# Kernel optimization log

Measured on AMD Instinct MI355X. Metric: run time of the kernel, lower is better.

The kernel has to match this reference:

```python
import jax, jax.numpy as jnp
import numpy as np

D_MODEL = 256
SELF_NHEAD = 8
ATT_NHEAD = 8
DFF = 1024
H2D, W2D = 40, 40
MAX_DIS = 7
WS = 2 * MAX_DIS + 1  # 15x15 local window
LOCAL_DIL = 1
GN_GROUPS = 32
EPS = 1e-5


def _ln(x, g, b):
    m = jnp.mean(x, -1, keepdims=True)
    v = jnp.var(x, -1, keepdims=True)
    return (x - m) * jax.lax.rsqrt(v + EPS) * g + b


def _mha_core(q, k, v, nh):
    # q,k,v: (L, B, C); Q scaled by 1/sqrt(head_dim) as in AOT MultiheadAttention
    Lq, B, C = q.shape
    hd = C // nh
    qh = (q / jnp.asarray(hd ** 0.5, q.dtype)).reshape(Lq, B, nh, hd).transpose(1, 2, 0, 3)
    kh = k.reshape(-1, B, nh, hd).transpose(1, 2, 0, 3)
    vh = v.reshape(-1, B, nh, hd).transpose(1, 2, 0, 3)
    attn = jax.nn.softmax(jnp.einsum('bhqd,bhkd->bhqk', qh, kh), axis=-1)
    o = jnp.einsum('bhqk,bhkd->bhqd', attn, vh)
    return o.transpose(2, 0, 1, 3).reshape(Lq, B, C)


def _unfold(x, ws, dil):
    # x: (N, C, H, W) -> (N, C, ws*ws, H, W) local windows (zero-padded)
    n, c, h, w = x.shape
    p = (ws // 2) * dil
    pat = jax.lax.conv_general_dilated_patches(
        x, (ws, ws), (1, 1), [(p, p), (p, p)], rhs_dilation=(dil, dil))
    return pat.reshape(n, c, ws * ws, h, w)


def _local_attn(q2, k2, v2, nh, ws, dil):
    # q2,k2,v2: (B, C, H, W); windowed attention over (2*max_dis+1)^2 neighborhood
    b, c, h, w = q2.shape
    hd = c // nh
    qh = (q2 / jnp.asarray(hd ** 0.5, q2.dtype)).reshape(b, nh, hd, h * w)
    uk = _unfold(k2, ws, dil).reshape(b, nh, hd, ws * ws, h * w)
    uv = _unfold(v2, ws, dil).reshape(b, nh, hd, ws * ws, h * w)
    valid = _unfold(jnp.ones((1, 1, h, w), q2.dtype), ws, dil).reshape(1, 1, ws * ws, h * w) > 0.5
    logits = jnp.einsum('bhdn,bhdwn->bhwn', qh, uk)
    logits = jnp.where(valid, logits, jnp.asarray(-1e9, logits.dtype))
    attn = jax.nn.softmax(logits, axis=2)
    o = jnp.einsum('bhwn,bhdwn->bhdn', attn, uv)
    return o.reshape(b, c, h * w).transpose(2, 0, 1)  # (HW, B, C)


def _seq_to_2d(x, h, w):
    l, b, c = x.shape
    return x.reshape(h, w, b, c).transpose(2, 3, 0, 1)  # (B, C, h, w)


def _block(tgt, curr_id_emb, self_pos,
           ln1_g, ln1_b, sa_wq, sa_bq, sa_wk, sa_bk, sa_wv, sa_bv, sa_wo, sa_bo,
           ln2_g, ln2_b, w_qv, b_qv, w_id, b_id, lt_wo, lt_bo, st_wo, st_bo,
           ln3_g, ln3_b, w1, b1, gn_g, gn_b, dw_k, w2, b2):
    h, w = H2D, W2D
    # --- self attention (global_dilation == 1) ---
    _t = _ln(tgt, ln1_g, ln1_b)
    qk_in = _t + self_pos
    q_ = qk_in @ sa_wq.T + sa_bq
    k_ = qk_in @ sa_wk.T + sa_bk
    v_ = _t @ sa_wv.T + sa_bv
    tgt2 = _mha_core(q_, k_, v_, SELF_NHEAD) @ sa_wo.T + sa_bo
    tgt = tgt + tgt2
    # --- QV projection + ID-gated KV fusion ---
    _t = _ln(tgt, ln2_g, ln2_b)
    qv = _t @ w_qv.T + b_qv
    curr_Q = qv[..., :D_MODEL]  # curr_K == curr_Q
    curr_V = qv[..., D_MODEL:]
    id_kv = curr_id_emb @ w_id.T + b_id
    id_k = id_kv[..., :ATT_NHEAD]
    id_v = id_kv[..., ATT_NHEAD:]
    L, B, C = curr_Q.shape
    hd = C // ATT_NHEAD
    global_K = (curr_Q.reshape(L, B, ATT_NHEAD, hd) * (1.0 + jnp.tanh(id_k))[..., None]).reshape(L, B, C)
    global_V = curr_V + id_v
    # --- long-term (global) attention, no input linear ---
    tgt2 = _mha_core(curr_Q, global_K, global_V, ATT_NHEAD) @ lt_wo.T + lt_bo
    # --- short-term (local windowed) attention ---
    lq = _seq_to_2d(curr_Q, h, w)
    lk = _seq_to_2d(global_K, h, w)
    lv = _seq_to_2d(global_V, h, w)
    tgt3 = _local_attn(lq, lk, lv, ATT_NHEAD, WS, LOCAL_DIL) @ st_wo.T + st_bo
    tgt = tgt + tgt2 + tgt3
    # --- FFN with GN + GELU + depthwise 5x5 conv (GNActDWConv2d) ---
    _t = _ln(tgt, ln3_g, ln3_b)
    x = _t @ w1.T + b1  # (L, B, DFF)
    x2 = _seq_to_2d(x, h, w)  # (B, DFF, h, w)
    xr = x2.reshape(B, GN_GROUPS, DFF // GN_GROUPS, h, w)
    m = xr.mean((2, 3, 4), keepdims=True)
    va = xr.var((2, 3, 4), keepdims=True)
    x2 = ((xr - m) * jax.lax.rsqrt(va + EPS)).reshape(B, DFF, h, w)
    x2 = x2 * gn_g[None, :, None, None] + gn_b[None, :, None, None]
    x2 = jax.nn.gelu(x2, approximate=False)
    x2 = jax.lax.conv_general_dilated(
        x2, dw_k, (1, 1), [(2, 2), (2, 2)], feature_group_count=DFF,
        dimension_numbers=('NCHW', 'OIHW', 'NCHW'))
    x = x2.reshape(B, DFF, h * w).transpose(2, 0, 1)
    tgt2 = x @ w2.T + b2
    return tgt + tgt2


def setup_inputs() -> dict:
    key = jax.random.key(0)
    ks = jax.random.split(key, 40)
    L = H2D * W2D
    B = 1
    C = D_MODEL
    w = lambda k, s: jax.random.normal(k, s, jnp.float32) * 0.02
    inp = {
        'tgt': jax.random.normal(ks[0], (L, B, C), jnp.float32),
        'curr_id_emb': jax.random.normal(ks[1], (L, B, C), jnp.float32),
        'self_pos': jax.random.normal(ks[2], (L, B, C), jnp.float32),
        'ln1_g': jnp.ones((C,), jnp.float32), 'ln1_b': jnp.zeros((C,), jnp.float32),
        'sa_wq': w(ks[3], (C, C)), 'sa_bq': jnp.zeros((C,), jnp.float32),
        'sa_wk': w(ks[4], (C, C)), 'sa_bk': jnp.zeros((C,), jnp.float32),
        'sa_wv': w(ks[5], (C, C)), 'sa_bv': jnp.zeros((C,), jnp.float32),
        'sa_wo': w(ks[6], (C, C)), 'sa_bo': jnp.zeros((C,), jnp.float32),
        'ln2_g': jnp.ones((C,), jnp.float32), 'ln2_b': jnp.zeros((C,), jnp.float32),
        'w_qv': w(ks[7], (2 * C, C)), 'b_qv': jnp.zeros((2 * C,), jnp.float32),
        'w_id': w(ks[8], (C + ATT_NHEAD, C)), 'b_id': jnp.zeros((C + ATT_NHEAD,), jnp.float32),
        'lt_wo': w(ks[9], (C, C)), 'lt_bo': jnp.zeros((C,), jnp.float32),
        'st_wo': w(ks[10], (C, C)), 'st_bo': jnp.zeros((C,), jnp.float32),
        'ln3_g': jnp.ones((C,), jnp.float32), 'ln3_b': jnp.zeros((C,), jnp.float32),
        'w1': w(ks[11], (DFF, C)), 'b1': jnp.zeros((DFF,), jnp.float32),
        'gn_g': jnp.ones((DFF,), jnp.float32), 'gn_b': jnp.zeros((DFF,), jnp.float32),
        'dw_k': w(ks[12], (DFF, 1, 5, 5)),
        'w2': w(ks[13], (C, DFF)), 'b2': jnp.zeros((C,), jnp.float32),
    }
    return inp


def reference(tgt, curr_id_emb, self_pos,
              ln1_g, ln1_b, sa_wq, sa_bq, sa_wk, sa_bk, sa_wv, sa_bv, sa_wo, sa_bo,
              ln2_g, ln2_b, w_qv, b_qv, w_id, b_id, lt_wo, lt_bo, st_wo, st_bo,
              ln3_g, ln3_b, w1, b1, gn_g, gn_b, dw_k, w2, b2):
    return _block(tgt, curr_id_emb, self_pos,
                  ln1_g, ln1_b, sa_wq, sa_bq, sa_wk, sa_bk, sa_wv, sa_bv, sa_wo, sa_bo,
                  ln2_g, ln2_b, w_qv, b_qv, w_id, b_id, lt_wo, lt_bo, st_wo, st_bo,
                  ln3_g, ln3_b, w1, b1, gn_g, gn_b, dw_k, w2, b2)
```

## Files before the change

### kernel.cpp

```cpp
#include <hip/hip_runtime.h>
#include <math.h>

#define L_SEQ 1600
#define CDIM 256
#define NH 8
#define HD 32
#define GRID_H 40
#define GRID_W 40
#define DFF_ 1024
#define SCALE_QK 0.17677669529663687f

typedef __attribute__((ext_vector_type(8))) short short8;
typedef __attribute__((ext_vector_type(4))) float f32x4;

__device__ __forceinline__ float waveReduceSum(float v) {
#pragma unroll
    for (int off = 32; off > 0; off >>= 1) v += __shfl_down(v, off, 64);
    return v;
}
__device__ __forceinline__ float blockReduceSum(float v, float* sh4) {
    v = waveReduceSum(v);
    int lane = threadIdx.x & 63, wid = threadIdx.x >> 6;
    __syncthreads();
    if (lane == 0) sh4[wid] = v;
    __syncthreads();
    return sh4[0] + sh4[1] + sh4[2] + sh4[3];
}

__device__ __forceinline__ unsigned short f2bf(float x) {
    union { float f; unsigned u; } v; v.f = x;
    unsigned r = (v.u + 0x7FFFu + ((v.u >> 16) & 1u)) >> 16;
    return (unsigned short)r;
}
__device__ __forceinline__ unsigned pkbf(float lo, float hi) {
    return (unsigned)f2bf(lo) | ((unsigned)f2bf(hi) << 16);
}

__global__ __launch_bounds__(256) void ln_kernel(const float* __restrict__ x,
                                                 const float* __restrict__ g,
                                                 const float* __restrict__ b,
                                                 const float* __restrict__ addin,
                                                 float* __restrict__ out,
                                                 float* __restrict__ out2) {
    __shared__ float sh4[4];
    int row = blockIdx.x;
    int c = threadIdx.x;
    float v = x[row * CDIM + c];
    float mean = blockReduceSum(v, sh4) * (1.0f / CDIM);
    float d = v - mean;
    float var = blockReduceSum(d * d, sh4) * (1.0f / CDIM);
    float y = d * rsqrtf(var + 1e-5f) * g[c] + b[c];
    out[row * CDIM + c] = y;
    if (out2) out2[row * CDIM + c] = y + addin[row * CDIM + c];
}

struct GJob {
    const float* A; const float* W; const float* bias; const float* res;
    float* C; int N; int K;
};

__global__ __launch_bounds__(256) void gemm_mfma(GJob j0, GJob j1, GJob j2) {
    GJob j = j0;
    if (blockIdx.z == 1) j = j1;
    else if (blockIdx.z == 2) j = j2;
    const float* __restrict__ A = j.A;
    const float* __restrict__ W = j.W;
    const float* bias = j.bias;
    const float* res = j.res;
    float* __restrict__ C = j.C;
    int N = j.N, K = j.K;

    __shared__ unsigned short Al[2][4][64][8];
    __shared__ unsigned short Bl[2][4][64][8];
    int tid = threadIdx.x;
    int bm = blockIdx.y * 64, bn = blockIdx.x * 64;
    if (bn >= N) return;
    int lane = tid & 63, wave = tid >> 6;
    int wr = wave >> 1, wc = wave & 1;

    int srow = tid >> 3;
    int q = tid & 7;
    int e0 = (q & 1) * 4;

    f32x4 acc[2][2] = {};
    int nsteps = K >> 5;

    float4 ra[2], rb[2];
    {
#pragma unroll
        for (int r = 0; r < 2; ++r) {
            int row = srow + 32 * r;
            ra[r] = *(const float4*)(A + (bm + row) * K + 4 * q);
            int n = bn + row;
            rb[r] = (n < N) ? *(const float4*)(W + n * K + 4 * q)
                            : make_float4(0.f, 0.f, 0.f, 0.f);
        }
#pragma unroll
        for (int r = 0; r < 2; ++r) {
            int row = srow + 32 * r;
            int frag = (row >> 4), l = (row & 15) + 16 * (q >> 1);
            *(uint2*)&Al[0][frag][l][e0] = make_uint2(pkbf(ra[r].x, ra[r].y), pkbf(ra[r].z, ra[r].w));
            *(uint2*)&Bl[0][frag][l][e0] = make_uint2(pkbf(rb[r].x, rb[r].y), pkbf(rb[r].z, rb[r].w));
        }
    }
    __syncthreads();

    for (int s = 0; s < nsteps; ++s) {
        bool more = (s + 1) < nsteps;
        if (more) {
            int k0 = (s + 1) << 5;
#pragma unroll
            for (int r = 0; r < 2; ++r) {
                int row = srow + 32 * r;
                ra[r] = *(const float4*)(A + (bm + row) * K + k0 + 4 * q);
                int n = bn + row;
                rb[r] = (n < N) ? *(const float4*)(W + n * K + k0 + 4 * q)
                                : make_float4(0.f, 0.f, 0.f, 0.f);
            }
        }
        {
            int buf = s & 1;
            short8 af[2], bfr[2];
#pragma unroll
            for (int i = 0; i < 2; ++i) {
                af[i] = *(const short8*)&Al[buf][2 * wr + i][lane][0];
                bfr[i] = *(const short8*)&Bl[buf][2 * wc + i][lane][0];
            }
#pragma unroll
            for (int i = 0; i < 2; ++i)
#pragma unroll
                for (int jj = 0; jj < 2; ++jj)
                    acc[i][jj] = __builtin_amdgcn_mfma_f32_16x16x32_bf16(af[i], bfr[jj], acc[i][jj], 0, 0, 0);
        }
        if (more) {
            int buf = (s + 1) & 1;
#pragma unroll
            for (int r = 0; r < 2; ++r) {
                int row = srow + 32 * r;
                int frag = (row >> 4), l = (row & 15) + 16 * (q >> 1);
                *(uint2*)&Al[buf][frag][l][e0] = make_uint2(pkbf(ra[r].x, ra[r].y), pkbf(ra[r].z, ra[r].w));
                *(uint2*)&Bl[buf][frag][l][e0] = make_uint2(pkbf(rb[r].x, rb[r].y), pkbf(rb[r].z, rb[r].w));
            }
        }
        __syncthreads();
    }

#pragma unroll
    for (int jj = 0; jj < 2; ++jj) {
        int col = bn + wc * 32 + jj * 16 + (lane & 15);
        if (col >= N) continue;
        float bv = bias ? bias[col] : 0.f;
#pragma unroll
        for (int i = 0; i < 2; ++i) {
            int rbase = bm + wr * 32 + i * 16 + ((lane >> 4) << 2);
#pragma unroll
            for (int r = 0; r < 4; ++r) {
                int row = rbase + r;
                float v = acc[i][jj][r] + bv;
                if (res) v += res[row * N + col];
                C[row * N + col] = v;
            }
        }
    }
}

#define QBLK 32
#define KTJ 128
__global__ __launch_bounds__(256) void mha_mfma(const float* __restrict__ Q, int ldq,
                                                const float* __restrict__ K, int ldk,
                                                const float* __restrict__ V, int ldv,
                                                const float* __restrict__ idkv,
                                                float* __restrict__ O, int ldo) {
    __shared__ unsigned short Kl[8][64][8];
    __shared__ unsigned short Vl[4][2][64][12];
    __shared__ float mred[4][2][16];
    __shared__ float lred[4][2][16];
    __shared__ float Osh[3][2][2][64][4];
    int h = blockIdx.y;
    int qbase = blockIdx.x * QBLK;
    int tid = threadIdx.x;
    int w = tid >> 6, lane = tid & 63;
    int g = lane >> 4, c = lane & 15;

    short8 qfrag[2];
#pragma unroll
    for (int qt = 0; qt < 2; ++qt) {
        const float* qp = Q + (qbase + qt * 16 + c) * ldq + h * HD + g * 8;
        float4 f0 = *(const float4*)qp;
        float4 f1 = *(const float4*)(qp + 4);
        short8 s;
        s[0] = (short)f2bf(f0.x * SCALE_QK); s[1] = (short)f2bf(f0.y * SCALE_QK);
        s[2] = (short)f2bf(f0.z * SCALE_QK); s[3] = (short)f2bf(f0.w * SCALE_QK);
        s[4] = (short)f2bf(f1.x * SCALE_QK); s[5] = (short)f2bf(f1.y * SCALE_QK);
        s[6] = (short)f2bf(f1.z * SCALE_QK); s[7] = (short)f2bf(f1.w * SCALE_QK);
        qfrag[qt] = s;
    }

    float m[2] = { -INFINITY, -INFINITY };
    float l[2] = { 0.f, 0.f };
    f32x4 acc_o[2][2] = {};

    int jrow = tid >> 1;
    int dhalf = (tid & 1) * 16;
    int vjq = tid >> 3;
    int vdq = tid & 7;
    int vjr = 4 * vjq;
    int vd0 = 4 * vdq;
    int vjc = vjr >> 5, vdt = vd0 >> 4, vjg = (vjr & 31) >> 3, ve0 = vjr & 7;

    int src_lo = 16 * ((2 * g) & 3) + c;
    int src_hi = 16 * ((2 * g + 1) & 3) + c;
    bool hisel = (g >= 2);

    for (int t = 0; t < L_SEQ; t += KTJ) {
        {
            int jj = t + jrow;
            float4 f0, f1, f2, f3;
            if (jj < L_SEQ) {
                const float4* kp = (const float4*)(K + jj * ldk + h * HD + dhalf);
                f0 = kp[0]; f1 = kp[1]; f2 = kp[2]; f3 = kp[3];
                if (idkv) {
                    float gt = 1.f + tanhf(idkv[jj * 264 + h]);
                    f0.x *= gt; f0.y *= gt; f0.z *= gt; f0.w *= gt;
                    f1.x *= gt; f1.y *= gt; f1.z *= gt; f1.w *= gt;
                    f2.x *= gt; f2.y *= gt; f2.z *= gt; f2.w *= gt;
                    f3.x *= gt; f3.y *= gt; f3.z *= gt; f3.w *= gt;
                }
            } else {
                f0 = f1 = f2 = f3 = make_float4(0.f, 0.f, 0.f, 0.f);
            }
            int jt = jrow >> 4;
            int laneA = (jrow & 15) + dhalf * 2;
            short8 s0, s1;
            s0[0]=f2bf(f0.x); s0[1]=f2bf(f0.y); s0[2]=f2bf(f0.z); s0[3]=f2bf(f0.w);
            s0[4]=f2bf(f1.x); s0[5]=f2bf(f1.y); s0[6]=f2bf(f1.z); s0[7]=f2bf(f1.w);
            s1[0]=f2bf(f2.x); s1[1]=f2bf(f2.y); s1[2]=f2bf(f2.z); s1[3]=f2bf(f2.w);
            s1[4]=f2bf(f3.x); s1[5]=f2bf(f3.y); s1[6]=f2bf(f3.z); s1[7]=f2bf(f3.w);
            *(short8*)&Kl[jt][laneA][0] = s0;
            *(short8*)&Kl[jt][laneA + 16][0] = s1;
        }
        {
            float4 rr[4];
            int j0 = t + vjr;
#pragma unroll
            for (int r = 0; r < 4; ++r) {
                int jj = j0 + r;
                if (jj < L_SEQ) {
                    float4 fv = *(const float4*)(V + jj * ldv + h * HD + vd0);
                    if (idkv) {
                        float4 av = *(const float4*)(idkv + jj * 264 + 8 + h * HD + vd0);
                        fv.x += av.x; fv.y += av.y; fv.z += av.z; fv.w += av.w;
                    }
                    rr[r] = fv;
                } else {
                    rr[r] = make_float4(0.f, 0.f, 0.f, 0.f);
                }
            }
            float col[4][4] = {
                { rr[0].x, rr[1].x, rr[2].x, rr[3].x },
                { rr[0].y, rr[1].y, rr[2].y, rr[3].y },
                { rr[0].z, rr[1].z, rr[2].z, rr[3].z },
                { rr[0].w, rr[1].w, rr[2].w, rr[3].w } };
#pragma unroll
            for (int dd = 0; dd < 4; ++dd) {
                int laneV = ((vd0 + dd) & 15) + 16 * vjg;
                uint2 pk;
                pk.x = pkbf(col[dd][0], col[dd][1]);
                pk.y = pkbf(col[dd][2], col[dd][3]);
                *(uint2*)&Vl[vjc][vdt][laneV][ve0] = pk;
            }
        }
        __syncthreads();

        bool alive = (t + 32 * w) < L_SEQ;
        if (alive) {
            short8 kf0 = *(const short8*)&Kl[2 * w][lane][0];
            short8 kf1 = *(const short8*)&Kl[2 * w + 1][lane][0];
            f32x4 zero = { 0.f, 0.f, 0.f, 0.f };
            f32x4 s[2][2];
            s[0][0] = __builtin_amdgcn_mfma_f32_16x16x32_bf16(kf0, qfrag[0], zero, 0, 0, 0);
            s[0][1] = __builtin_amdgcn_mfma_f32_16x16x32_bf16(kf0, qfrag[1], zero, 0, 0, 0);
            s[1][0] = __builtin_amdgcn_mfma_f32_16x16x32_bf16(kf1, qfrag[0], zero, 0, 0, 0);
            s[1][1] = __builtin_amdgcn_mfma_f32_16x16x32_bf16(kf1, qfrag[1], zero, 0, 0, 0);

            short8 pfrag[2];
#pragma unroll
            for (int qt = 0; qt < 2; ++qt) {
                float mx = s[0][qt][0];
                mx = fmaxf(mx, s[0][qt][1]); mx = fmaxf(mx, s[0][qt][2]); mx = fmaxf(mx, s[0][qt][3]);
                mx = fmaxf(mx, s[1][qt][0]); mx = fmaxf(mx, s[1][qt][1]);
                mx = fmaxf(mx, s[1][qt][2]); mx = fmaxf(mx, s[1][qt][3]);
                mx = fmaxf(mx, __shfl_xor(mx, 16, 64));
                mx = fmaxf(mx, __shfl_xor(mx, 32, 64));
                float nm = fmaxf(m[qt], mx);
                float alpha = __expf(m[qt] - nm);
                m[qt] = nm;
                float p00 = __expf(s[0][qt][0] - nm), p01 = __expf(s[0][qt][1] - nm);
                float p02 = __expf(s[0][qt][2] - nm), p03 = __expf(s[0][qt][3] - nm);
                float p10 = __expf(s[1][qt][0] - nm), p11 = __expf(s[1][qt][1] - nm);
                float p12 = __expf(s[1][qt][2] - nm), p13 = __expf(s[1][qt][3] - nm);
                float ts = ((p00 + p01) + (p02 + p03)) + ((p10 + p11) + (p12 + p13));
                ts += __shfl_xor(ts, 16, 64);
                ts += __shfl_xor(ts, 32, 64);
                l[qt] = l[qt] * alpha + ts;
#pragma unroll
                for (int dt = 0; dt < 2; ++dt) {
                    acc_o[dt][qt][0] *= alpha; acc_o[dt][qt][1] *= alpha;
                    acc_o[dt][qt][2] *= alpha; acc_o[dt][qt][3] *= alpha;
                }
                unsigned w00 = pkbf(p00, p01), w01 = pkbf(p02, p03);
                unsigned w10 = pkbf(p10, p11), w11 = pkbf(p12, p13);
                unsigned a0 = __shfl(w00, src_lo, 64);
                unsigned a1 = __shfl(w10, src_lo, 64);
                unsigned b0 = __shfl(w01, src_lo, 64);
                unsigned b1 = __shfl(w11, src_lo, 64);
                unsigned c0 = __shfl(w00, src_hi, 64);
                unsigned c1 = __shfl(w10, src_hi, 64);
                unsigned d0 = __shfl(w01, src_hi, 64);
                unsigned d1 = __shfl(w11, src_hi, 64);
                union { short8 s8; unsigned u[4]; } P;
                P.u[0] = hisel ? a1 : a0;
                P.u[1] = hisel ? b1 : b0;
                P.u[2] = hisel ? c1 : c0;
                P.u[3] = hisel ? d1 : d0;
                pfrag[qt] = P.s8;
            }

            union { short8 s8; uint2 v[2]; } vf0u, vf1u;
            vf0u.v[0] = *(const uint2*)&Vl[w][0][lane][0];
            vf0u.v[1] = *(const uint2*)&Vl[w][0][lane][4];
            vf1u.v[0] = *(const uint2*)&Vl[w][1][lane][0];
            vf1u.v[1] = *(const uint2*)&Vl[w][1][lane][4];
            acc_o[0][0] = __builtin_amdgcn_mfma_f32_16x16x32_bf16(vf0u.s8, pfrag[0], acc_o[0][0], 0, 0, 0);
            acc_o[0][1] = __builtin_amdgcn_mfma_f32_16x16x32_bf16(vf0u.s8, pfrag[1], acc_o[0][1], 0, 0, 0);
            acc_o[1][0] = __builtin_amdgcn_mfma_f32_16x16x32_bf16(vf1u.s8, pfrag[0], acc_o[1][0], 0, 0, 0);
            acc_o[1][1] = __builtin_amdgcn_mfma_f32_16x16x32_bf16(vf1u.s8, pfrag[1], acc_o[1][1], 0, 0, 0);
        }
        __syncthreads();
    }

    if (g == 0) {
#pragma unroll
        for (int qt = 0; qt < 2; ++qt) { mred[w][qt][c] = m[qt]; lred[w][qt][c] = l[qt]; }
    }
    if (w > 0) {
#pragma unroll
        for (int dt = 0; dt < 2; ++dt)
#pragma unroll
            for (int qt = 0; qt < 2; ++qt)
                *(f32x4*)&Osh[w - 1][dt][qt][lane][0] = acc_o[dt][qt];
    }
    __syncthreads();
    if (w == 0) {
#pragma unroll
        for (int qt = 0; qt < 2; ++qt) {
            float m0_ = mred[0][qt][c], m1_ = mred[1][qt][c];
            float m2_ = mred[2][qt][c], m3_ = mred[3][qt][c];
            float M = fmaxf(fmaxf(m0_, m1_), fmaxf(m2_, m3_));
            float a0 = __expf(m0_ - M), a1 = __expf(m1_ - M);
            float a2 = __expf(m2_ - M), a3 = __expf(m3_ - M);
            float L = a0 * lred[0][qt][c] + a1 * lred[1][qt][c]
                    + a2 * lred[2][qt][c] + a3 * lred[3][qt][c];
            float inv = 1.f / L;
#pragma unroll
            for (int dt = 0; dt < 2; ++dt) {
                f32x4 o1 = *(const f32x4*)&Osh[0][dt][qt][lane][0];
                f32x4 o2 = *(const f32x4*)&Osh[1][dt][qt][lane][0];
                f32x4 o3 = *(const f32x4*)&Osh[2][dt][qt][lane][0];
                float4 r;
                r.x = (acc_o[dt][qt][0] * a0 + o1[0] * a1 + o2[0] * a2 + o3[0] * a3) * inv;
                r.y = (acc_o[dt][qt][1] * a0 + o1[1] * a1 + o2[1] * a2 + o3[1] * a3) * inv;
                r.z = (acc_o[dt][qt][2] * a0 + o1[2] * a1 + o2[2] * a2 + o3[2] * a3) * inv;
                r.w = (acc_o[dt][qt][3] * a0 + o1[3] * a1 + o2[3] * a2 + o3[3] * a3) * inv;
                *(float4*)(O + (qbase + qt * 16 + c) * ldo + h * HD + dt * 16 + 4 * g) = r;
            }
        }
    }
}

__global__ __launch_bounds__(256, 1) void local_mfma(const float* __restrict__ Q, int ldq,
                                                     const float* __restrict__ K, int ldk,
                                                     const float* __restrict__ V, int ldv,
                                                     const float* __restrict__ idkv,
                                                     float* __restrict__ O, int ldo) {
    __shared__ unsigned short Kp[768 * 40];
    __shared__ unsigned short Vt[32 * 776];
    __shared__ float mred[4][3][16];
    __shared__ float lred[4][3][16];
    __shared__ float Osh[3][2][3][64][4];
    int y = blockIdx.x, h = blockIdx.y;
    int tid = threadIdx.x;
    int w = tid >> 6, lane = tid & 63;
    int g = lane >> 4, c = lane & 15;

#pragma unroll 4
    for (int rep = 0; rep < 24; ++rep) {
        int idx = rep * 256 + tid;
        int key = idx >> 3, dq = idx & 7;
        int ky = key / 48;
        int xx = key - 48 * ky;
        int yy = y + ky - 7;
        bool ok = (xx < 40) && (yy >= 0) && (yy < 40);
        float4 fk = make_float4(0.f, 0.f, 0.f, 0.f);
        float4 fv = make_float4(0.f, 0.f, 0.f, 0.f);
        if (ok) {
            int row = yy * 40 + xx;
            fk = *(const float4*)(K + row * ldk + h * HD + 4 * dq);
            fv = *(const float4*)(V + row * ldv + h * HD + 4 * dq);
            if (idkv) {
                float gt = 1.f + tanhf(idkv[row * 264 + h]);
                fk.x *= gt; fk.y *= gt; fk.z *= gt; fk.w *= gt;
                float4 av = *(const float4*)(idkv + row * 264 + 8 + h * HD + 4 * dq);
                fv.x += av.x; fv.y += av.y; fv.z += av.z; fv.w += av.w;
            }
        }
        *(uint2*)&Kp[key * 40 + 4 * dq] = make_uint2(pkbf(fk.x, fk.y), pkbf(fk.z, fk.w));
        int vb = (4 * dq) * 776 + key;
        Vt[vb] = f2bf(fv.x);
        Vt[vb + 776] = f2bf(fv.y);
        Vt[vb + 1552] = f2bf(fv.z);
        Vt[vb + 2328] = f2bf(fv.w);
    }

    short8 qfrag[3];
#pragma unroll
    for (int qt = 0; qt < 3; ++qt) {
        short8 s = { 0, 0, 0, 0, 0, 0, 0, 0 };
        int qx = qt * 16 + c;
        if (qx < 40) {
            const float* qp = Q + (y * 40 + qx) * ldq + h * HD + g * 8;
            float4 f0 = *(const float4*)qp;
            float4 f1 = *(const float4*)(qp + 4);
            s[0] = (short)f2bf(f0.x * SCALE_QK); s[1] = (short)f2bf(f0.y * SCALE_QK);
            s[2] = (short)f2bf(f0.z * SCALE_QK); s[3] = (short)f2bf(f0.w * SCALE_QK);
            s[4] = (short)f2bf(f1.x * SCALE_QK); s[5] = (short)f2bf(f1.y * SCALE_QK);
            s[6] = (short)f2bf(f1.z * SCALE_QK); s[7] = (short)f2bf(f1.w * SCALE_QK);
        }
        qfrag[qt] = s;
    }
    __syncthreads();

    f32x4 sfr[12][3];
    const f32x4 zf = { 0.f, 0.f, 0.f, 0.f };
#pragma unroll
    for (int i = 0; i < 12; ++i) {
        int ky = 4 * w + i / 3;
        int fx = i % 3;
        short8 kf = *(const short8*)&Kp[(ky * 48 + fx * 16 + c) * 40 + 8 * g];
#pragma unroll
        for (int qt = 0; qt < 3; ++qt)
            sfr[i][qt] = __builtin_amdgcn_mfma_f32_16x16x32_bf16(kf, qfrag[qt], zf, 0, 0, 0);
    }

    float mw[3] = { -1e30f, -1e30f, -1e30f };
#pragma unroll
    for (int i = 0; i < 12; ++i) {
        int ky = 4 * w + i / 3, fx = i % 3;
        int yy = y + ky - 7;
        bool rowok = (yy >= 0) && (yy < 40);
        int xxb = fx * 16 + 4 * g;
#pragma unroll
        for (int qt = 0; qt < 3; ++qt) {
            int qx = qt * 16 + c;
#pragma unroll
            for (int r = 0; r < 4; ++r) {
                int xx = xxb + r;
                int dd = xx - qx;
                bool ok = rowok && (xx < 40) && (dd <= 7) && (dd >= -7);
                float v = ok ? sfr[i][qt][r] : -1e9f;
                sfr[i][qt][r] = v;
                mw[qt] = fmaxf(mw[qt], v);
            }
        }
    }
#pragma unroll
    for (int qt = 0; qt < 3; ++qt) {
        mw[qt] = fmaxf(mw[qt], __shfl_xor(mw[qt], 16, 64));
        mw[qt] = fmaxf(mw[qt], __shfl_xor(mw[qt], 32, 64));
    }
    if (lane < 16) {
#pragma unroll
        for (int qt = 0; qt < 3; ++qt) mred[w][qt][lane] = mw[qt];
    }
    __syncthreads();
    float M[3];
#pragma unroll
    for (int qt = 0; qt < 3; ++qt)
        M[qt] = fmaxf(fmaxf(mred[0][qt][c], mred[1][qt][c]),
                      fmaxf(mred[2][qt][c], mred[3][qt][c]));

    float lsum[3] = { 0.f, 0.f, 0.f };
    f32x4 acc_o[2][3] = {};
    int src_lo = 16 * ((2 * g) & 3) + c;
    int src_hi = 16 * ((2 * g + 1) & 3) + c;
    bool hisel = (g >= 2);
#pragma unroll
    for (int chk = 0; chk < 6; ++chk) {
        short8 pfrag[3];
#pragma unroll
        for (int qt = 0; qt < 3; ++qt) {
            float p00 = __expf(sfr[2 * chk][qt][0] - M[qt]);
            float p01 = __expf(sfr[2 * chk][qt][1] - M[qt]);
            float p02 = __expf(sfr[2 * chk][qt][2] - M[qt]);
            float p03 = __expf(sfr[2 * chk][qt][3] - M[qt]);
            float p10 = __expf(sfr[2 * chk + 1][qt][0] - M[qt]);
            float p11 = __expf(sfr[2 * chk + 1][qt][1] - M[qt]);
            float p12 = __expf(sfr[2 * chk + 1][qt][2] - M[qt]);
            float p13 = __expf(sfr[2 * chk + 1][qt][3] - M[qt]);
            lsum[qt] += ((p00 + p01) + (p02 + p03)) + ((p10 + p11) + (p12 + p13));
            unsigned w00 = pkbf(p00, p01), w01 = pkbf(p02, p03);
            unsigned w10 = pkbf(p10, p11), w11 = pkbf(p12, p13);
            unsigned a0 = __shfl(w00, src_lo, 64);
            unsigned a1 = __shfl(w10, src_lo, 64);
            unsigned b0 = __shfl(w01, src_lo, 64);
            unsigned b1 = __shfl(w11, src_lo, 64);
            unsigned c0 = __shfl(w00, src_hi, 64);
            unsigned c1 = __shfl(w10, src_hi, 64);
            unsigned d0 = __shfl(w01, src_hi, 64);
            unsigned d1 = __shfl(w11, src_hi, 64);
            union { short8 s8; unsigned u[4]; } P;
            P.u[0] = hisel ? a1 : a0;
            P.u[1] = hisel ? b1 : b0;
            P.u[2] = hisel ? c1 : c0;
            P.u[3] = hisel ? d1 : d0;
            pfrag[qt] = P.s8;
        }
        int jb = 32 * (6 * w + chk);
        short8 vf0 = *(const short8*)&Vt[c * 776 + jb + 8 * g];
        short8 vf1 = *(const short8*)&Vt[(16 + c) * 776 + jb + 8 * g];
#pragma unroll
        for (int qt = 0; qt < 3; ++qt) {
            acc_o[0][qt] = __builtin_amdgcn_mfma_f32_16x16x32_bf16(vf0, pfrag[qt], acc_o[0][qt], 0, 0, 0);
            acc_o[1][qt] = __builtin_amdgcn_mfma_f32_16x16x32_bf16(vf1, pfrag[qt], acc_o[1][qt], 0, 0, 0);
        }
    }

#pragma unroll
    for (int qt = 0; qt < 3; ++qt) {
        lsum[qt] += __shfl_xor(lsum[qt], 16, 64);
        lsum[qt] += __shfl_xor(lsum[qt], 32, 64);
    }
    if (lane < 16) {
#pragma unroll
        for (int qt = 0; qt < 3; ++qt) lred[w][qt][lane] = lsum[qt];
    }
    if (w > 0) {
#pragma unroll
        for (int dt = 0; dt < 2; ++dt)
#pragma unroll
            for (int qt = 0; qt < 3; ++qt)
                *(f32x4*)&Osh[w - 1][dt][qt][lane][0] = acc_o[dt][qt];
    }
    __syncthreads();
    if (w == 0) {
#pragma unroll
        for (int qt = 0; qt < 3; ++qt) {
            int qx = qt * 16 + c;
            if (qx >= 40) continue;
            float L = (lred[0][qt][c] + lred[1][qt][c]) + (lred[2][qt][c] + lred[3][qt][c]);
            float inv = 1.f / L;
#pragma unroll
            for (int dt = 0; dt < 2; ++dt) {
                f32x4 o1 = *(const f32x4*)&Osh[0][dt][qt][lane][0];
                f32x4 o2 = *(const f32x4*)&Osh[1][dt][qt][lane][0];
                f32x4 o3 = *(const f32x4*)&Osh[2][dt][qt][lane][0];
                float4 r;
                r.x = (acc_o[dt][qt][0] + o1[0] + o2[0] + o3[0]) * inv;
                r.y = (acc_o[dt][qt][1] + o1[1] + o2[1] + o3[1]) * inv;
                r.z = (acc_o[dt][qt][2] + o1[2] + o2[2] + o3[2]) * inv;
                r.w = (acc_o[dt][qt][3] + o1[3] + o2[3] + o3[3]) * inv;
                *(float4*)(O + (y * 40 + qx) * ldo + h * HD + dt * 16 + 4 * g) = r;
            }
        }
    }
}

__global__ __launch_bounds__(256) void prep_misc(const float* __restrict__ Kw,
                                                 const float* __restrict__ lt_wo,
                                                 const float* __restrict__ lt_bo,
                                                 const float* __restrict__ st_wo,
                                                 const float* __restrict__ st_bo,
                                                 float* __restrict__ Kt,
                                                 float* __restrict__ wcat,
                                                 float* __restrict__ bsum) {
    int idx = blockIdx.x * 256 + threadIdx.x;
    int n = idx >> 8, k = idx & 255;
    wcat[n * 512 + k] = lt_wo[idx];
    wcat[n * 512 + 256 + k] = st_wo[idx];
    if (idx < 256) bsum[idx] = lt_bo[idx] + st_bo[idx];
    if (idx < 25 * DFF_) {
        int kk = idx >> 10, c = idx & 1023;
        Kt[idx] = Kw[c * 25 + kk];
    }
}

__global__ __launch_bounds__(256) void gn_partial(const float* __restrict__ X,
                                                  float* __restrict__ gstat) {
    __shared__ float sh4[4];
    int g = blockIdx.x, chunk = blockIdx.y;
    int base = g * 32;
    float s = 0.f, s2 = 0.f;
    for (int i = threadIdx.x; i < 200 * 32; i += 256) {
        int l = chunk * 200 + (i >> 5), c = i & 31;
        float v = X[l * DFF_ + base + c];
        s += v;
        s2 += v * v;
    }
    s = blockReduceSum(s, sh4);
    s2 = blockReduceSum(s2, sh4);
    if (threadIdx.x == 0) {
        gstat[g * 8 + chunk] = s;
        gstat[256 + g * 8 + chunk] = s2;
    }
}

__global__ __launch_bounds__(256) void gn_apply(const float* __restrict__ X,
                                                const float* __restrict__ gstat,
                                                const float* __restrict__ g,
                                                const float* __restrict__ b,
                                                float* __restrict__ Y) {
    int idx = blockIdx.x * 256 + threadIdx.x;
    int e4 = idx * 4;
    int c = e4 & 1023;
    int grp = c >> 5;
    float s = 0.f, s2 = 0.f;
#pragma unroll
    for (int i = 0; i < 8; ++i) {
        s += gstat[grp * 8 + i];
        s2 += gstat[256 + grp * 8 + i];
    }
    const float invn = 1.0f / 51200.f;
    float mean = s * invn;
    float rs = rsqrtf(s2 * invn - mean * mean + 1e-5f);
    float4 v = *(const float4*)(X + e4);
    float4 gg = *(const float4*)(g + c);
    float4 bb = *(const float4*)(b + c);
    float4 r;
    float y0 = (v.x - mean) * rs * gg.x + bb.x;
    float y1 = (v.y - mean) * rs * gg.y + bb.y;
    float y2 = (v.z - mean) * rs * gg.z + bb.z;
    float y3 = (v.w - mean) * rs * gg.w + bb.w;
    r.x = 0.5f * y0 * (1.0f + erff(y0 * 0.70710678118654752f));
    r.y = 0.5f * y1 * (1.0f + erff(y1 * 0.70710678118654752f));
    r.z = 0.5f * y2 * (1.0f + erff(y2 * 0.70710678118654752f));
    r.w = 0.5f * y3 * (1.0f + erff(y3 * 0.70710678118654752f));
    *(float4*)(Y + e4) = r;
}

__global__ __launch_bounds__(256) void dwconv_v2(const float* __restrict__ X,
                                                 const float* __restrict__ Kt,
                                                 float* __restrict__ Y) {
    int l = blockIdx.x;
    int c4 = threadIdx.x * 4;
    int y = l / GRID_W, x = l - y * GRID_W;
    float4 acc = make_float4(0.f, 0.f, 0.f, 0.f);
    if (y >= 2 && y < GRID_H - 2 && x >= 2 && x < GRID_W - 2) {
#pragma unroll
        for (int ky = 0; ky < 5; ++ky) {
#pragma unroll
            for (int kx = 0; kx < 5; ++kx) {
                float4 xv = *(const float4*)(X + ((y + ky - 2) * GRID_W + x + kx - 2) * DFF_ + c4);
                float4 wv = *(const float4*)(Kt + (ky * 5 + kx) * DFF_ + c4);
                acc.x += xv.x * wv.x; acc.y += xv.y * wv.y;
                acc.z += xv.z * wv.z; acc.w += xv.w * wv.w;
            }
        }
    } else {
#pragma unroll
        for (int ky = 0; ky < 5; ++ky) {
            int yy = y + ky - 2;
            if (yy < 0 || yy >= GRID_H) continue;
#pragma unroll
            for (int kx = 0; kx < 5; ++kx) {
                int xx = x + kx - 2;
                if (xx < 0 || xx >= GRID_W) continue;
                float4 xv = *(const float4*)(X + (yy * GRID_W + xx) * DFF_ + c4);
                float4 wv = *(const float4*)(Kt + (ky * 5 + kx) * DFF_ + c4);
                acc.x += xv.x * wv.x; acc.y += xv.y * wv.y;
                acc.z += xv.z * wv.z; acc.w += xv.w * wv.w;
            }
        }
    }
    *(float4*)(Y + l * DFF_ + c4) = acc;
}

extern "C" void kernel_launch(void* const* d_in, const int* in_sizes, int n_in,
                              void* d_out, int out_size, void* d_ws, size_t ws_size,
                              hipStream_t stream) {
    (void)in_sizes; (void)n_in; (void)out_size; (void)ws_size;
    const float* tgt = (const float*)d_in[0];
    const float* curr_id_emb = (const float*)d_in[1];
    const float* self_pos = (const float*)d_in[2];
    const float* ln1_g = (const float*)d_in[3];
    const float* ln1_b = (const float*)d_in[4];
    const float* sa_wq = (const float*)d_in[5];
    const float* sa_bq = (const float*)d_in[6];
    const float* sa_wk = (const float*)d_in[7];
    const float* sa_bk = (const float*)d_in[8];
    const float* sa_wv = (const float*)d_in[9];
    const float* sa_bv = (const float*)d_in[10];
    const float* sa_wo = (const float*)d_in[11];
    const float* sa_bo = (const float*)d_in[12];
    const float* ln2_g = (const float*)d_in[13];
    const float* ln2_b = (const float*)d_in[14];
    const float* w_qv = (const float*)d_in[15];
    const float* b_qv = (const float*)d_in[16];
    const float* w_id = (const float*)d_in[17];
    const float* b_id = (const float*)d_in[18];
    const float* lt_wo = (const float*)d_in[19];
    const float* lt_bo = (const float*)d_in[20];
    const float* st_wo = (const float*)d_in[21];
    const float* st_bo = (const float*)d_in[22];
    const float* ln3_g = (const float*)d_in[23];
    const float* ln3_b = (const float*)d_in[24];
    const float* w1 = (const float*)d_in[25];
    const float* b1 = (const float*)d_in[26];
    const float* gn_g = (const float*)d_in[27];
    const float* gn_b = (const float*)d_in[28];
    const float* dw_k = (const float*)d_in[29];
    const float* w2 = (const float*)d_in[30];
    const float* b2 = (const float*)d_in[31];
    float* out = (float*)d_out;

    float* ws = (float*)d_ws;
    const int LC = L_SEQ * CDIM;
    float* bufA = ws;
    float* bufB = bufA + LC;
    float* bufC = bufB + LC;
    float* bufD = bufC + LC;
    float* bufE = bufD + LC;
    float* bufG = bufE + LC;
    float* bufFW = bufG + LC;
    float* bufH = bufFW + L_SEQ * 512;
    float* bufI = bufH + L_SEQ * 512;
    float* bufX = bufI + L_SEQ * 264;
    float* bufY = bufX + L_SEQ * DFF_;
    float* bufZ = bufY + L_SEQ * DFF_;
    float* bufW = bufZ + L_SEQ * DFF_;
    float* wcat = bufW + 25 * DFF_;
    float* bsum = wcat + 256 * 512;

    dim3 blk(256);
    dim3 mhaGrid(L_SEQ / QBLK, NH);
    auto J = [](const float* A, const float* W, const float* bias, const float* res,
                float* C, int N, int K) {
        GJob j; j.A = A; j.W = W; j.bias = bias; j.res = res; j.C = C; j.N = N; j.K = K;
        return j;
    };

    prep_misc<<<256, blk, 0, stream>>>(dw_k, lt_wo, lt_bo, st_wo, st_bo, bufW, wcat, bsum);
    ln_kernel<<<L_SEQ, blk, 0, stream>>>(tgt, ln1_g, ln1_b, self_pos, bufA, bufB);
    {
        GJob jq = J(bufB, sa_wq, sa_bq, nullptr, bufC, CDIM, CDIM);
        GJob jk = J(bufB, sa_wk, sa_bk, nullptr, bufD, CDIM, CDIM);
        GJob jv = J(bufA, sa_wv, sa_bv, nullptr, bufE, CDIM, CDIM);
        gemm_mfma<<<dim3(4, 25, 3), blk, 0, stream>>>(jq, jk, jv);
    }
    mha_mfma<<<mhaGrid, blk, 0, stream>>>(bufC, CDIM, bufD, CDIM, bufE, CDIM, nullptr, bufFW, CDIM);
    {
        GJob jo = J(bufFW, sa_wo, sa_bo, tgt, bufG, CDIM, CDIM);
        gemm_mfma<<<dim3(4, 25, 1), blk, 0, stream>>>(jo, jo, jo);
    }
    ln_kernel<<<L_SEQ, blk, 0, stream>>>(bufG, ln2_g, ln2_b, nullptr, bufA, nullptr);
    {
        GJob jqv = J(bufA, w_qv, b_qv, nullptr, bufH, 512, CDIM);
        GJob jid = J(curr_id_emb, w_id, b_id, nullptr, bufI, 264, CDIM);
        gemm_mfma<<<dim3(8, 25, 2), blk, 0, stream>>>(jqv, jid, jid);
    }
    mha_mfma<<<mhaGrid, blk, 0, stream>>>(bufH, 512, bufH, 512, bufH + 256, 512, bufI, bufFW, 512);
    local_mfma<<<dim3(GRID_H, NH), blk, 0, stream>>>(bufH, 512, bufH, 512, bufH + 256, 512, bufI, bufFW + 256, 512);
    {
        GJob jm = J(bufFW, wcat, bsum, bufG, bufB, CDIM, 512);
        gemm_mfma<<<dim3(4, 25, 1), blk, 0, stream>>>(jm, jm, jm);
    }
    ln_kernel<<<L_SEQ, blk, 0, stream>>>(bufB, ln3_g, ln3_b, nullptr, bufA, nullptr);
    {
        GJob jw1 = J(bufA, w1, b1, nullptr, bufX, DFF_, CDIM);
        gemm_mfma<<<dim3(16, 25, 1), blk, 0, stream>>>(jw1, jw1, jw1);
    }
    gn_partial<<<dim3(32, 8), blk, 0, stream>>>(bufX, bufH);
    gn_apply<<<L_SEQ, blk, 0, stream>>>(bufX, bufH, gn_g, gn_b, bufY);
    dwconv_v2<<<L_SEQ, blk, 0, stream>>>(bufY, bufW, bufZ);
    {
        GJob jw2 = J(bufZ, w2, b2, bufB, out, CDIM, DFF_);
        gemm_mfma<<<dim3(4, 25, 1), blk, 0, stream>>>(jw2, jw2, jw2);
    }
}
```

Baseline: 377.5 us.

## Precompute bf16 MFMA-layout K/V tiles once in a prep kernel for MHA

Adds a prep_kv kernel that applies the ID gating and value offset to K/V once, converts them to bf16, and writes them in the exact shared-memory fragment layout. The attention kernel then streams these tiles with plain float4 copies instead of redoing the conversion, gating and transpose in each of its 50 query blocks per head. This removes redundant fp32 loads and conversion work, at the cost of an extra launch and an extra round trip through global memory for the packed buffers.

```diff
diff --git a/kernel.cpp b/kernel.cpp
--- a/kernel.cpp
+++ b/kernel.cpp
@@ -9,6 +9,7 @@
 #define GRID_W 40
 #define DFF_ 1024
 #define SCALE_QK 0.17677669529663687f
+#define NTILE 13
 
 typedef __attribute__((ext_vector_type(8))) short short8;
 typedef __attribute__((ext_vector_type(4))) float f32x4;
@@ -164,12 +165,85 @@
     }
 }
 
+#define KTJ 128
+__global__ __launch_bounds__(256) void prep_kv(const float* __restrict__ K, int ldk,
+                                               const float* __restrict__ V, int ldv,
+                                               const float* __restrict__ idkv,
+                                               unsigned short* __restrict__ Kf,
+                                               unsigned short* __restrict__ Vf) {
+    int tile = blockIdx.x, h = blockIdx.y;
+    int t = tile * KTJ;
+    int tid = threadIdx.x;
+    unsigned short* kb = Kf + (h * NTILE + tile) * 4096;
+    unsigned short* vb = Vf + (h * NTILE + tile) * 6144;
+    {
+        int jrow = tid >> 1;
+        int dhalf = (tid & 1) * 16;
+        int jj = t + jrow;
+        float4 f0, f1, f2, f3;
+        if (jj < L_SEQ) {
+            const float4* kp = (const float4*)(K + jj * ldk + h * HD + dhalf);
+            f0 = kp[0]; f1 = kp[1]; f2 = kp[2]; f3 = kp[3];
+            if (idkv) {
+                float gt = 1.f + tanhf(idkv[jj * 264 + h]);
+                f0.x *= gt; f0.y *= gt; f0.z *= gt; f0.w *= gt;
+                f1.x *= gt; f1.y *= gt; f1.z *= gt; f1.w *= gt;
+                f2.x *= gt; f2.y *= gt; f2.z *= gt; f2.w *= gt;
+                f3.x *= gt; f3.y *= gt; f3.z *= gt; f3.w *= gt;
+            }
+        } else {
+            f0 = f1 = f2 = f3 = make_float4(0.f, 0.f, 0.f, 0.f);
+        }
+        int jt = jrow >> 4;
+        int laneA = (jrow & 15) + dhalf * 2;
+        short8 s0, s1;
+        s0[0]=f2bf(f0.x); s0[1]=f2bf(f0.y); s0[2]=f2bf(f0.z); s0[3]=f2bf(f0.w);
+        s0[4]=f2bf(f1.x); s0[5]=f2bf(f1.y); s0[6]=f2bf(f1.z); s0[7]=f2bf(f1.w);
+        s1[0]=f2bf(f2.x); s1[1]=f2bf(f2.y); s1[2]=f2bf(f2.z); s1[3]=f2bf(f2.w);
+        s1[4]=f2bf(f3.x); s1[5]=f2bf(f3.y); s1[6]=f2bf(f3.z); s1[7]=f2bf(f3.w);
+        *(short8*)&kb[(jt * 64 + laneA) * 8] = s0;
+        *(short8*)&kb[(jt * 64 + laneA + 16) * 8] = s1;
+    }
+    {
+        int vjq = tid >> 3, vdq = tid & 7;
+        int vjr = 4 * vjq, vd0 = 4 * vdq;
+        int vjc = vjr >> 5, vdt = vd0 >> 4, vjg = (vjr & 31) >> 3, ve0 = vjr & 7;
+        float4 rr[4];
+        int j0 = t + vjr;
+#pragma unroll
+        for (int r = 0; r < 4; ++r) {
+            int jj = j0 + r;
+            if (jj < L_SEQ) {
+                float4 fv = *(const float4*)(V + jj * ldv + h * HD + vd0);
+                if (idkv) {
+                    float4 av = *(const float4*)(idkv + jj * 264 + 8 + h * HD + vd0);
+                    fv.x += av.x; fv.y += av.y; fv.z += av.z; fv.w += av.w;
+                }
+                rr[r] = fv;
+            } else {
+                rr[r] = make_float4(0.f, 0.f, 0.f, 0.f);
+            }
+        }
+        float col[4][4] = {
+            { rr[0].x, rr[1].x, rr[2].x, rr[3].x },
+            { rr[0].y, rr[1].y, rr[2].y, rr[3].y },
+            { rr[0].z, rr[1].z, rr[2].z, rr[3].z },
+            { rr[0].w, rr[1].w, rr[2].w, rr[3].w } };
+#pragma unroll
+        for (int dd = 0; dd < 4; ++dd) {
+            int laneV = ((vd0 + dd) & 15) + 16 * vjg;
+            uint2 pk;
+            pk.x = pkbf(col[dd][0], col[dd][1]);
+            pk.y = pkbf(col[dd][2], col[dd][3]);
+            *(uint2*)&vb[((vjc * 2 + vdt) * 64 + laneV) * 12 + ve0] = pk;
+        }
+    }
+}
+
 #define QBLK 32
-#define KTJ 128
 __global__ __launch_bounds__(256) void mha_mfma(const float* __restrict__ Q, int ldq,
-                                                const float* __restrict__ K, int ldk,
-                                                const float* __restrict__ V, int ldv,
-                                                const float* __restrict__ idkv,
+                                                const unsigned short* __restrict__ Kf,
+                                                const unsigned short* __restrict__ Vf,
                                                 float* __restrict__ O, int ldo) {
     __shared__ unsigned short Kl[8][64][8];
     __shared__ unsigned short Vl[4][2][64][12];
@@ -200,75 +274,25 @@
     float l[2] = { 0.f, 0.f };
     f32x4 acc_o[2][2] = {};
 
-    int jrow = tid >> 1;
-    int dhalf = (tid & 1) * 16;
-    int vjq = tid >> 3;
-    int vdq = tid & 7;
-    int vjr = 4 * vjq;
-    int vd0 = 4 * vdq;
-    int vjc = vjr >> 5, vdt = vd0 >> 4, vjg = (vjr & 31) >> 3, ve0 = vjr & 7;
-
     int src_lo = 16 * ((2 * g) & 3) + c;
     int src_hi = 16 * ((2 * g + 1) & 3) + c;
     bool hisel = (g >= 2);
 
-    for (int t = 0; t < L_SEQ; t += KTJ) {
+    const float4* kfb = (const float4*)(Kf + h * NTILE * 4096);
+    const float4* vfb = (const float4*)(Vf + h * NTILE * 6144);
+    float4* kdst = (float4*)&Kl[0][0][0];
+    float4* vdst = (float4*)&Vl[0][0][0][0];
+
+    for (int tile = 0; tile < NTILE; ++tile) {
+        int t = tile * KTJ;
         {
-            int jj = t + jrow;
-            float4 f0, f1, f2, f3;
-            if (jj < L_SEQ) {
-                const float4* kp = (const float4*)(K + jj * ldk + h * HD + dhalf);
-                f0 = kp[0]; f1 = kp[1]; f2 = kp[2]; f3 = kp[3];
-                if (idkv) {
-                    float gt = 1.f + tanhf(idkv[jj * 264 + h]);
-                    f0.x *= gt; f0.y *= gt; f0.z *= gt; f0.w *= gt;
-                    f1.x *= gt; f1.y *= gt; f1.z *= gt; f1.w *= gt;
-                    f2.x *= gt; f2.y *= gt; f2.z *= gt; f2.w *= gt;
-                    f3.x *= gt; f3.y *= gt; f3.z *= gt; f3.w *= gt;
-                }
-            } else {
-                f0 = f1 = f2 = f3 = make_float4(0.f, 0.f, 0.f, 0.f);
-            }
-            int jt = jrow >> 4;
-            int laneA = (jrow & 15) + dhalf * 2;
-            short8 s0, s1;
-            s0[0]=f2bf(f0.x); s0[1]=f2bf(f0.y); s0[2]=f2bf(f0.z); s0[3]=f2bf(f0.w);
-            s0[4]=f2bf(f1.x); s0[5]=f2bf(f1.y); s0[6]=f2bf(f1.z); s0[7]=f2bf(f1.w);
-            s1[0]=f2bf(f2.x); s1[1]=f2bf(f2.y); s1[2]=f2bf(f2.z); s1[3]=f2bf(f2.w);
-            s1[4]=f2bf(f3.x); s1[5]=f2bf(f3.y); s1[6]=f2bf(f3.z); s1[7]=f2bf(f3.w);
-            *(short8*)&Kl[jt][laneA][0] = s0;
-            *(short8*)&Kl[jt][laneA + 16][0] = s1;
-        }
-        {
-            float4 rr[4];
-            int j0 = t + vjr;
-#pragma unroll
-            for (int r = 0; r < 4; ++r) {
-                int jj = j0 + r;
-                if (jj < L_SEQ) {
-                    float4 fv = *(const float4*)(V + jj * ldv + h * HD + vd0);
-                    if (idkv) {
-                        float4 av = *(const float4*)(idkv + jj * 264 + 8 + h * HD + vd0);
-                        fv.x += av.x; fv.y += av.y; fv.z += av.z; fv.w += av.w;
-                    }
-                    rr[r] = fv;
-                } else {
-                    rr[r] = make_float4(0.f, 0.f, 0.f, 0.f);
-                }
-            }
-            float col[4][4] = {
-                { rr[0].x, rr[1].x, rr[2].x, rr[3].x },
-                { rr[0].y, rr[1].y, rr[2].y, rr[3].y },
-                { rr[0].z, rr[1].z, rr[2].z, rr[3].z },
-                { rr[0].w, rr[1].w, rr[2].w, rr[3].w } };
-#pragma unroll
-            for (int dd = 0; dd < 4; ++dd) {
-                int laneV = ((vd0 + dd) & 15) + 16 * vjg;
-                uint2 pk;
-                pk.x = pkbf(col[dd][0], col[dd][1]);
-                pk.y = pkbf(col[dd][2], col[dd][3]);
-                *(uint2*)&Vl[vjc][vdt][laneV][ve0] = pk;
-            }
+            const float4* ks = kfb + tile * 512;
+            const float4* vs = vfb + tile * 768;
+            kdst[tid] = ks[tid];
+            kdst[tid + 256] = ks[tid + 256];
+            vdst[tid] = vs[tid];
+            vdst[tid + 256] = vs[tid + 256];
+            vdst[tid + 512] = vs[tid + 512];
         }
         __syncthreads();
 
@@ -739,9 +763,12 @@
     float* bufW = bufZ + L_SEQ * DFF_;
     float* wcat = bufW + 25 * DFF_;
     float* bsum = wcat + 256 * 512;
+    unsigned short* Kf = (unsigned short*)(bsum + 256);
+    unsigned short* Vf = Kf + NH * NTILE * 4096;
 
     dim3 blk(256);
     dim3 mhaGrid(L_SEQ / QBLK, NH);
+    dim3 prepGrid(NTILE, NH);
     auto J = [](const float* A, const float* W, const float* bias, const float* res,
                 float* C, int N, int K) {
         GJob j; j.A = A; j.W = W; j.bias = bias; j.res = res; j.C = C; j.N = N; j.K = K;
@@ -756,7 +783,8 @@
         GJob jv = J(bufA, sa_wv, sa_bv, nullptr, bufE, CDIM, CDIM);
         gemm_mfma<<<dim3(4, 25, 3), blk, 0, stream>>>(jq, jk, jv);
     }
-    mha_mfma<<<mhaGrid, blk, 0, stream>>>(bufC, CDIM, bufD, CDIM, bufE, CDIM, nullptr, bufFW, CDIM);
+    prep_kv<<<prepGrid, blk, 0, stream>>>(bufD, CDIM, bufE, CDIM, nullptr, Kf, Vf);
+    mha_mfma<<<mhaGrid, blk, 0, stream>>>(bufC, CDIM, Kf, Vf, bufFW, CDIM);
     {
         GJob jo = J(bufFW, sa_wo, sa_bo, tgt, bufG, CDIM, CDIM);
         gemm_mfma<<<dim3(4, 25, 1), blk, 0, stream>>>(jo, jo, jo);
@@ -767,7 +795,8 @@
         GJob jid = J(curr_id_emb, w_id, b_id, nullptr, bufI, 264, CDIM);
         gemm_mfma<<<dim3(8, 25, 2), blk, 0, stream>>>(jqv, jid, jid);
     }
-    mha_mfma<<<mhaGrid, blk, 0, stream>>>(bufH, 512, bufH, 512, bufH + 256, 512, bufI, bufFW, 512);
+    prep_kv<<<prepGrid, blk, 0, stream>>>(bufH, 512, bufH + 256, 512, bufI, Kf, Vf);
+    mha_mfma<<<mhaGrid, blk, 0, stream>>>(bufH, 512, Kf, Vf, bufFW, 512);
     local_mfma<<<dim3(GRID_H, NH), blk, 0, stream>>>(bufH, 512, bufH, 512, bufH + 256, 512, bufI, bufFW + 256, 512);
     {
         GJob jm = J(bufFW, wcat, bsum, bufG, bufB, CDIM, 512);
```

New measurement: 354.9 us. 6.0% less time.
